# Optimization experiments

Measured on AMD Instinct MI355X. Metric: run time of the kernel, lower is better.

## Reference

```python
import jax, jax.numpy as jnp
import numpy as np

G, N, H = 64, 512, 64          # graphs, nodes/graph, hidden
NT = G * N                     # total nodes
DEG = 32
ET = NT * DEG                  # total edges
KP = int(np.ceil(0.7 * N))     # TopKPooling keep per graph (359)
NP2 = G * KP                   # nodes after pooling
F_IN, NC, NA = 128, 2, 6
seg = jax.ops.segment_sum


def graph_norm(h, batch, num_g, w, b, ms, eps=1e-5):
    cnt = seg(jnp.ones((h.shape[0], 1), h.dtype), batch, num_segments=num_g)
    mean = seg(h, batch, num_segments=num_g) / cnt
    hc = h - ms * mean[batch]
    var = seg(hc * hc, batch, num_segments=num_g) / cnt
    return w * hc / jnp.sqrt(var[batch] + eps) + b


def sage(h, src, tgt, valid, Ws, Wn, b, n_nodes):
    # PyG SAGEConv (mean aggr): out_i = x_i@Ws + mean_{j->i} x_j @ Wn + b
    msg = h[src] * valid[:, None]
    agg = seg(msg, tgt, num_segments=n_nodes)
    deg = seg(valid, tgt, num_segments=n_nodes)
    return h @ Ws + (agg / jnp.maximum(deg, 1.0)[:, None]) @ Wn + b


def setup_inputs() -> dict:
    key = jax.random.key(0)
    ks = jax.random.split(key, 20)
    offs = (jnp.arange(G) * N)[:, None]
    src = (jax.random.randint(ks[0], (G, N * DEG), 0, N) + offs).reshape(-1)
    tgt = (jax.random.randint(ks[1], (G, N * DEG), 0, N) + offs).reshape(-1)
    edge_index = jnp.stack([src, tgt])  # within-graph edges

    def lin(k, fi, fo):
        return jax.random.normal(k, (fi, fo), jnp.float32) / np.sqrt(fi)

    return {
        "x": jax.random.normal(ks[2], (NT, F_IN), jnp.float32),
        "edge_index": edge_index,
        "edge_attr": jax.random.uniform(ks[3], (ET,), jnp.float32),
        "coords": jax.random.normal(ks[4], (NT, 3), jnp.float32),
        "anatomical_class": jax.random.randint(ks[5], (NT,), 0, NA),
        "Bk_table": jax.random.normal(ks[6], (NA, H * H), jnp.float32) * 0.05,
        "pos_W": lin(ks[7], 3, H), "pos_b": jnp.zeros((H,), jnp.float32),
        "W1_self": lin(ks[8], F_IN, H), "W1_neigh": lin(ks[9], F_IN, H),
        "b1": jnp.zeros((H,), jnp.float32),
        "gn1_w": jnp.ones((H,), jnp.float32), "gn1_b": jnp.zeros((H,), jnp.float32),
        "gn1_ms": jnp.ones((H,), jnp.float32),
        "pool_p": jax.random.normal(ks[10], (H,), jnp.float32),
        "W2_self": lin(ks[11], H, H), "W2_neigh": lin(ks[12], H, H),
        "b2": jnp.zeros((H,), jnp.float32),
        "gn2_w": jnp.ones((H,), jnp.float32), "gn2_b": jnp.zeros((H,), jnp.float32),
        "gn2_ms": jnp.ones((H,), jnp.float32),
        "lin1_W": lin(ks[13], 3 * H, H), "lin1_b": jnp.zeros((H,), jnp.float32),
        "lin2_W": lin(ks[14], H, NC), "lin2_b": jnp.zeros((NC,), jnp.float32),
    }


def reference(x, edge_index, edge_attr, coords, anatomical_class, Bk_table,
              pos_W, pos_b, W1_self, W1_neigh, b1, gn1_w, gn1_b, gn1_ms,
              pool_p, W2_self, W2_neigh, b2, gn2_w, gn2_b, gn2_ms,
              lin1_W, lin1_b, lin2_W, lin2_b):
    row, col = edge_index[0], edge_index[1]
    batch = jnp.repeat(jnp.arange(G), N)
    # ---- stage 1: anatomical propagation kernel ----
    e = coords @ pos_W + pos_b                                 # [NT, H]
    Ae = seg(edge_attr[:, None] * e[col], row, num_segments=NT)  # SpMM adj @ e
    Bk = Bk_table[anatomical_class].reshape(NT, H, H)
    delta = jnp.einsum('nd,nhd->nh', Ae, Bk)                   # bmm(Ae, Bk^T)
    ones_e = jnp.ones((ET,), x.dtype)
    h = sage(x, row, col, ones_e, W1_self, W1_neigh, b1, NT)
    h = jax.nn.elu(graph_norm(h, batch, G, gn1_w, gn1_b, gn1_ms))
    h = h + delta
    h = jnp.einsum('nij,nj->ni', Bk + delta[:, :, None], h)    # propagate_message
    # ---- TopK pooling (equal-sized graphs) ----
    score = (h @ pool_p) / jnp.linalg.norm(pool_p)
    vals, idx = jax.lax.top_k(score.reshape(G, N), KP)
    perm = (idx + (jnp.arange(G) * N)[:, None]).reshape(-1)    # [NP2]
    h = h[perm] * jnp.tanh(vals).reshape(-1)[:, None]
    batch2 = jnp.repeat(jnp.arange(G), KP)
    node_map = jnp.full((NT,), -1, jnp.int32).at[perm].set(jnp.arange(NP2, dtype=jnp.int32))
    s2, t2 = node_map[row], node_map[col]
    valid = ((s2 >= 0) & (t2 >= 0)).astype(h.dtype)            # masked edge filter
    s2 = jnp.where(s2 >= 0, s2, 0)
    t2 = jnp.where(t2 >= 0, t2, 0)
    # ---- stage 2 ----
    e2 = coords[perm] @ pos_W + pos_b
    Bk2 = Bk_table[anatomical_class[perm]].reshape(NP2, H, H)
    Ae2 = seg(valid[:, None] * e2[t2], s2, num_segments=NP2)   # edge_attr = ones
    delta2 = jnp.einsum('nd,nhd->nh', Ae2, Bk2)
    h = h + delta2
    h = jnp.einsum('nij,nj->ni', Bk2 + delta2[:, :, None], h)
    h = sage(h, s2, t2, valid, W2_self, W2_neigh, b2, NP2)
    h = jax.nn.elu(graph_norm(h, batch2, G, gn2_w, gn2_b, gn2_ms))
    # ---- readout ----
    cnt = seg(jnp.ones((NP2, 1), h.dtype), batch2, num_segments=G)
    hsum = seg(h, batch2, num_segments=G)
    g = jnp.concatenate([hsum / cnt,
                         jax.ops.segment_max(h, batch2, num_segments=G),
                         hsum], axis=1)
    g = jax.nn.relu(g @ lin1_W + lin1_b)
    return jax.nn.log_softmax(g @ lin2_W + lin2_b, axis=1)
```

## Files before the change

### kernel.cpp

```cpp
#include <hip/hip_runtime.h>
#include <math.h>

#define G_    64
#define N_    512
#define NT_   32768
#define ET_   1048576
#define EPG_  16384
#define KP_   359
#define NP2_  22976
#define FIN_  128

__device__ __forceinline__
void gemm_unit(int unit, const float* __restrict__ in, int K,
               const float* __restrict__ Wa, const float* __restrict__ Wb,
               const float* __restrict__ bias,
               float* __restrict__ outA, float* __restrict__ outB,
               float* inT, int t) {
    int row0 = unit * 32;
    for (int idx = t; idx < 32 * K; idx += 256) inT[idx] = in[row0 * K + idx];
    __syncthreads();
    int c = t & 63, rb = t >> 6;
    const float* ip = inT + (rb * 8) * K;
    float aA[8] = {0,0,0,0,0,0,0,0};
    float aB[8] = {0,0,0,0,0,0,0,0};
    for (int k = 0; k < K; k += 4) {
        float wa0 = Wa[(k+0)*64 + c], wa1 = Wa[(k+1)*64 + c];
        float wa2 = Wa[(k+2)*64 + c], wa3 = Wa[(k+3)*64 + c];
        float wb0 = Wb[(k+0)*64 + c], wb1 = Wb[(k+1)*64 + c];
        float wb2 = Wb[(k+2)*64 + c], wb3 = Wb[(k+3)*64 + c];
        #pragma unroll
        for (int r = 0; r < 8; r++) {
            float4 xv = *(const float4*)&ip[r*K + k];
            aA[r] += xv.x*wa0; aB[r] += xv.x*wb0;
            aA[r] += xv.y*wa1; aB[r] += xv.y*wb1;
            aA[r] += xv.z*wa2; aB[r] += xv.z*wb2;
            aA[r] += xv.w*wa3; aB[r] += xv.w*wb3;
        }
    }
    float bv = bias[c];
    #pragma unroll
    for (int r = 0; r < 8; r++) {
        int node = row0 + rb*8 + r;
        outA[node*64 + c] = aA[r];
        outB[node*64 + c] = aB[r] + bv;
    }
}

__global__ __launch_bounds__(256)
void k_pregemm(const float* __restrict__ x,
               const float* __restrict__ W1n, const float* __restrict__ W1s,
               const float* __restrict__ b1,
               float* __restrict__ y, float* __restrict__ hself,
               const int* __restrict__ row, const int* __restrict__ col,
               int* __restrict__ histR8, int* __restrict__ histC8,
               const float* __restrict__ Bk, const float* __restrict__ posW,
               const float* __restrict__ posb,
               float* __restrict__ BkT, float* __restrict__ PT) {
    __shared__ float smem[32 * FIN_];
    int b = blockIdx.x, t = threadIdx.x;
    if (b < NT_/32) {
        gemm_unit(b, x, FIN_, W1n, W1s, b1, y, hself, smem, t);
    } else if (b < NT_/32 + 512) {
        int bb = b - NT_/32;
        int* hr = (int*)smem; int* hc = hr + N_;
        int g = bb >> 3, s = bb & 7;
        for (int i = t; i < N_; i += 256) { hr[i] = 0; hc[i] = 0; }
        __syncthreads();
        int ebase = g * EPG_ + s * 2048;
        for (int i = t; i < 2048; i += 256) {
            atomicAdd(&hr[row[ebase + i] & (N_ - 1)], 1);
            atomicAdd(&hc[col[ebase + i] & (N_ - 1)], 1);
        }
        __syncthreads();
        int sbase = bb * N_;
        for (int i = t; i < N_; i += 256) {
            histR8[sbase + i] = hr[i];
            histC8[sbase + i] = hc[i];
        }
    } else if (b < NT_/32 + 608) {
        int idx = (b - NT_/32 - 512) * 256 + t;
        int c = idx >> 12, r = idx & 4095;
        int h = r >> 6, d = r & 63;
        BkT[c*4096 + d*64 + h] = Bk[c*4096 + h*64 + d];
    } else {
        int c = b - (NT_/32 + 608);
        int i = t >> 6, h = t & 63;
        const float* B = Bk + c*4096 + h*64;
        float acc = 0.f;
        for (int d = 0; d < 64; d++) {
            float vd = (i < 3) ? posW[i*64 + d] : posb[d];
            acc += B[d] * vd;
        }
        PT[c*256 + i*64 + h] = acc;
    }
}

__global__ __launch_bounds__(1024)
void k_scatscan(const int* __restrict__ row, const int* __restrict__ col,
                const float* __restrict__ ea,
                const int* __restrict__ histR8, const int* __restrict__ histC8,
                int2* __restrict__ rowcsr, int* __restrict__ colcsr,
                int* __restrict__ rowptr, int* __restrict__ colptr,
                int* __restrict__ nmap) {
    __shared__ int hr[N_], hc[N_];
    int g = blockIdx.x >> 2, q = blockIdx.x & 3;
    int t = threadIdx.x;
    int lo = q * 128;
    int nbase = g * N_, ebase = g * EPG_;
    for (int i = t; i < N_; i += 1024) {
        int sr = 0, sc = 0;
        #pragma unroll
        for (int s = 0; s < 8; s++) {
            sr += histR8[(g*8 + s)*N_ + i];
            sc += histC8[(g*8 + s)*N_ + i];
        }
        hr[i] = sr; hc[i] = sc;
    }
    __syncthreads();
    int wave = t >> 6, lane = t & 63;
    if (wave < 2) {
        int* h = wave ? hc : hr;
        int base8 = lane * 8;
        int loc[8];
        int tot = 0;
        #pragma unroll
        for (int i = 0; i < 8; i++) { int v = h[base8 + i]; loc[i] = tot; tot += v; }
        int pref = tot;
        for (int off = 1; off < 64; off <<= 1) {
            int u = __shfl_up(pref, off);
            if (lane >= off) pref += u;
        }
        pref -= tot;
        #pragma unroll
        for (int i = 0; i < 8; i++) h[base8 + i] = pref + loc[i];
    }
    __syncthreads();
    if (t < 128) {
        int i = lo + t;
        rowptr[nbase + i] = ebase + hr[i];
        colptr[nbase + i] = ebase + hc[i];
        nmap[nbase + i] = -1;
    }
    if (blockIdx.x == 0 && t == 0) { rowptr[NT_] = ET_; colptr[NT_] = ET_; }
    __syncthreads();
    for (int i = t; i < EPG_; i += 1024) {
        int rg = row[ebase + i];
        int cg = col[ebase + i];
        int rl = (rg & (N_ - 1)) - lo;
        if ((unsigned)rl < 128u) {
            int pr = atomicAdd(&hr[lo + rl], 1);
            rowcsr[ebase + pr] = make_int2(cg, __float_as_int(ea[ebase + i]));
        }
        int cl = (cg & (N_ - 1)) - lo;
        if ((unsigned)cl < 128u) {
            int pc = atomicAdd(&hc[lo + cl], 1);
            colcsr[ebase + pc] = rg;
        }
    }
}

__global__ __launch_bounds__(256)
void k_edge1f(const int* __restrict__ rowptr, const int2* __restrict__ rcsr,
              const int* __restrict__ colptr, const int* __restrict__ ccsr,
              const float* __restrict__ coords, const float* __restrict__ y,
              const float* __restrict__ hself,
              float4* __restrict__ nsum, float* __restrict__ vbuf) {
    int node = blockIdx.x * 4 + (threadIdx.x >> 6);
    int lane = threadIdx.x & 63;
    int rs = rowptr[node], re = rowptr[node + 1];
    float sx = 0.f, sy = 0.f, sz = 0.f, sw = 0.f;
    for (int k = rs + lane; k < re; k += 64) {
        int2 ent = rcsr[k];
        int c = ent.x;
        float w = __int_as_float(ent.y);
        sx += w * coords[c*3+0];
        sy += w * coords[c*3+1];
        sz += w * coords[c*3+2];
        sw += w;
    }
    #pragma unroll
    for (int off = 32; off; off >>= 1) {
        sx += __shfl_xor(sx, off); sy += __shfl_xor(sy, off);
        sz += __shfl_xor(sz, off); sw += __shfl_xor(sw, off);
    }
    if (lane == 0) nsum[node] = make_float4(sx, sy, sz, sw);
    int cs = colptr[node], ce = colptr[node + 1];
    float acc = 0.f;
    #pragma unroll 8
    for (int k = cs; k < ce; k++) {
        int r = ccsr[k];
        acc += y[r*64 + lane];
    }
    vbuf[node*64 + lane] = hself[node*64 + lane] + acc / fmaxf((float)(ce - cs), 1.f);
}

__global__ __launch_bounds__(256)
void k_gnstat(const float* __restrict__ v, float* __restrict__ partial,
              int NPG, int CH, int npc) {
    __shared__ float r1[256], r2[256];
    int b = blockIdx.x;
    int g = b / CH, chunk = b % CH;
    int t = threadIdx.x, c = t & 63, grp = t >> 6;
    int n0 = chunk * npc;
    int nend = min(n0 + npc, NPG);
    float s1 = 0.f, s2 = 0.f;
    for (int n = n0 + grp; n < nend; n += 4) {
        float vv = v[(g * NPG + n)*64 + c];
        s1 += vv; s2 += vv * vv;
    }
    r1[t] = s1; r2[t] = s2;
    __syncthreads();
    if (grp == 0) {
        partial[b*128 + c]      = r1[c] + r1[64+c] + r1[128+c] + r1[192+c];
        partial[b*128 + 64 + c] = r2[c] + r2[64+c] + r2[128+c] + r2[192+c];
    }
}

__global__ __launch_bounds__(256)
void k_gnprop(const float* __restrict__ vbuf, const float* __restrict__ partial,
              const float* __restrict__ ms,
              const float* __restrict__ w, const float* __restrict__ b,
              const float4* __restrict__ nsum, const int* __restrict__ cls,
              const float* __restrict__ PT, const float* __restrict__ BkT,
              float* __restrict__ out) {
    __shared__ float hT[256];
    int t = threadIdx.x;
    int node = blockIdx.x * 4 + (t >> 6);
    int lane = t & 63;
    int g = (blockIdx.x * 4) >> 9;
    float s1 = 0.f, s2 = 0.f;
    #pragma unroll
    for (int i = 0; i < 8; i++) {
        s1 += partial[(g*8 + i)*128 + lane];
        s2 += partial[(g*8 + i)*128 + 64 + lane];
    }
    float m  = s1 / (float)N_, q = s2 / (float)N_, msv = ms[lane];
    float var = q - msv * m * m * (2.f - msv);
    float mval = msv * m;
    float istd = rsqrtf(var + 1e-5f);
    float4 s4 = nsum[node];
    int c = cls[node];
    const float* P = PT + c * 256;
    float d = s4.x*P[lane] + s4.y*P[64+lane] + s4.z*P[128+lane] + s4.w*P[192+lane];
    float v = vbuf[node*64 + lane];
    v = w[lane] * (v - mval) * istd + b[lane];
    v = v > 0.f ? v : expm1f(v);
    v += d;
    hT[t] = v;
    __syncthreads();
    float ssum = v;
    #pragma unroll
    for (int off = 32; off; off >>= 1) ssum += __shfl_xor(ssum, off);
    const float* B  = BkT + c * 4096;
    const float* hv = hT + (t & ~63);
    float acc = 0.f;
    #pragma unroll 8
    for (int j = 0; j < 64; j++) acc += B[j*64 + lane] * hv[j];
    out[node*64 + lane] = acc + d * ssum;
}

__global__ __launch_bounds__(512)
void k_topk(const float* __restrict__ hp, const float* __restrict__ p,
            const int* __restrict__ cls, const int* __restrict__ ccsr,
            const int* __restrict__ row, const int* __restrict__ col,
            int* __restrict__ perm, float* __restrict__ tanhv,
            int* __restrict__ node_map, int* __restrict__ class2,
            int* __restrict__ ccsr2, float* __restrict__ deg2) {
    __shared__ float key[N_];
    __shared__ int   idxS[N_];
    __shared__ int   lmap[N_];
    __shared__ int   ideg[KP_];
    __shared__ float pS[64];
    __shared__ float nrm;
    int g = blockIdx.x, t = threadIdx.x;
    lmap[t] = -1;
    if (t < 64) pS[t] = p[t];
    for (int i = t; i < KP_; i += 512) ideg[i] = 0;
    __syncthreads();
    if (t == 0) {
        float s = 0.f;
        for (int i = 0; i < 64; i++) s += pS[i] * pS[i];
        nrm = sqrtf(s);
    }
    __syncthreads();
    {
        float acc = 0.f;
        const float* hv = hp + (size_t)(g*N_ + t) * 64;
        for (int cdx = 0; cdx < 64; cdx++) acc += hv[cdx] * pS[cdx];
        key[t]  = acc / nrm;
        idxS[t] = t;
    }
    __syncthreads();
    for (int k = 2; k <= N_; k <<= 1) {
        for (int j = k >> 1; j > 0; j >>= 1) {
            int i = t, ixj = i ^ j;
            if (ixj > i) {
                float ki = key[i], kj = key[ixj];
                int   ii = idxS[i], ij = idxS[ixj];
                bool before = (ki > kj) || (ki == kj && ii < ij);
                bool dir = ((i & k) == 0);
                if (dir ? !before : before) {
                    key[i] = kj; key[ixj] = ki;
                    idxS[i] = ij; idxS[ixj] = ii;
                }
            }
            __syncthreads();
        }
    }
    if (t < KP_) {
        int orig  = idxS[t];
        int gnode = g * N_ + orig;
        int pj    = g * KP_ + t;
        perm[pj]     = gnode;
        tanhv[pj]    = tanhf(key[t]);
        node_map[gnode] = pj;
        class2[pj]   = cls[gnode];
        lmap[orig]   = pj;
    }
    __syncthreads();
    int ebase = g * EPG_;
    for (int k = t; k < EPG_; k += 512) {
        int mm = lmap[ccsr[ebase + k] & (N_ - 1)];
        ccsr2[ebase + k] = (mm >= 0) ? mm : NP2_;
    }
    for (int k = t; k < EPG_; k += 512) {
        int mr = lmap[row[ebase + k] & (N_ - 1)];
        int mc = lmap[col[ebase + k] & (N_ - 1)];
        if (mr >= 0 && mc >= 0) atomicAdd(&ideg[mc - g * KP_], 1);
    }
    __syncthreads();
    for (int i = t; i < KP_; i += 512) deg2[g * KP_ + i] = (float)ideg[i];
}

__global__ __launch_bounds__(256)
void k_s2prop(const int* __restrict__ rowptr, const int2* __restrict__ rcsr,
              const int* __restrict__ perm, const int* __restrict__ nmap,
              const float* __restrict__ coords,
              const float* __restrict__ hp, const float* __restrict__ tanhv,
              const int* __restrict__ cls2,
              const float* __restrict__ PT, const float* __restrict__ BkT,
              float* __restrict__ out, float* __restrict__ y2zero) {
    __shared__ float hT[256];
    int t = threadIdx.x;
    int j = blockIdx.x * 4 + (t >> 6);
    int lane = t & 63;
    if (blockIdx.x == 0 && t < 64) y2zero[t] = 0.f;
    int orig = perm[j];
    int rs = rowptr[orig], re = rowptr[orig + 1];
    float sx = 0.f, sy = 0.f, sz = 0.f, sw = 0.f;
    for (int k = rs + lane; k < re; k += 64) {
        int c = rcsr[k].x;
        if (nmap[c] >= 0) {
            sx += coords[c*3+0]; sy += coords[c*3+1]; sz += coords[c*3+2];
            sw += 1.f;
        }
    }
    #pragma unroll
    for (int off = 32; off; off >>= 1) {
        sx += __shfl_xor(sx, off); sy += __shfl_xor(sy, off);
        sz += __shfl_xor(sz, off); sw += __shfl_xor(sw, off);
    }
    int c = cls2[j];
    const float* P = PT + c * 256;
    float d = sx*P[lane] + sy*P[64+lane] + sz*P[128+lane] + sw*P[192+lane];
    float v = hp[orig*64 + lane] * tanhv[j] + d;
    hT[t] = v;
    __syncthreads();
    float ssum = v;
    #pragma unroll
    for (int off = 32; off; off >>= 1) ssum += __shfl_xor(ssum, off);
    const float* B  = BkT + c * 4096;
    const float* hv = hT + (t & ~63);
    float acc = 0.f;
    #pragma unroll 8
    for (int jj = 0; jj < 64; jj++) acc += B[jj*64 + lane] * hv[jj];
    out[j*64 + lane] = acc + d * ssum;
}

__global__ __launch_bounds__(256)
void k_gemm2(const float* __restrict__ in,
             const float* __restrict__ Wa, const float* __restrict__ Wb,
             const float* __restrict__ bias,
             float* __restrict__ outA, float* __restrict__ outB) {
    __shared__ float inT[32 * 64];
    gemm_unit(blockIdx.x, in, 64, Wa, Wb, bias, outA, outB, inT, threadIdx.x);
}

__global__ __launch_bounds__(256)
void k_gagg2v(const int* __restrict__ colptr, const int* __restrict__ ccsr2,
              const int* __restrict__ perm, const float* __restrict__ y2,
              const float* __restrict__ hs2, const float* __restrict__ deg2,
              float* __restrict__ v2buf) {
    int j = blockIdx.x * 4 + (threadIdx.x >> 6);
    int lane = threadIdx.x & 63;
    int orig = perm[j];
    int start = colptr[orig], end = colptr[orig + 1];
    float acc = 0.f;
    #pragma unroll 8
    for (int k = start; k < end; k++) {
        int r = ccsr2[k];
        acc += y2[r*64 + lane];
    }
    v2buf[j*64 + lane] = hs2[j*64 + lane] + acc / fmaxf(deg2[j], 1.f);
}

__global__ __launch_bounds__(256)
void k_gnrd(const float* __restrict__ v2, const float* __restrict__ statsP,
            const float* __restrict__ ms,
            const float* __restrict__ w, const float* __restrict__ b,
            float* __restrict__ readP) {
    __shared__ float r1[256], r2[256];
    int blk = blockIdx.x;
    int g = blk / 6, chunk = blk % 6;
    int t = threadIdx.x, c = t & 63, grp = t >> 6;
    float s1 = 0.f, s2 = 0.f;
    #pragma unroll
    for (int i = 0; i < 6; i++) {
        s1 += statsP[(g*6 + i)*128 + c];
        s2 += statsP[(g*6 + i)*128 + 64 + c];
    }
    float mean = s1 / (float)KP_, q = s2 / (float)KP_, msv = ms[c];
    float var = q - msv * mean * mean * (2.f - msv);
    float mv = msv * mean;
    float is = rsqrtf(var + 1e-5f);
    float wv = w[c], bv = b[c];
    int n0 = chunk * 60, nend = min(n0 + 60, KP_);
    float s = 0.f, m = -1e30f;
    for (int n = n0 + grp; n < nend; n += 4) {
        float v = v2[(g * KP_ + n)*64 + c];
        v = wv * (v - mv) * is + bv;
        v = v > 0.f ? v : expm1f(v);
        s += v; m = fmaxf(m, v);
    }
    r1[t] = s; r2[t] = m;
    __syncthreads();
    if (grp == 0) {
        readP[blk*128 + c]      = r1[c] + r1[64+c] + r1[128+c] + r1[192+c];
        readP[blk*128 + 64 + c] = fmaxf(fmaxf(r2[c], r2[64+c]), fmaxf(r2[128+c], r2[192+c]));
    }
}

__global__ void k_rfin(const float* __restrict__ part, int CH,
                       const float* __restrict__ l1W, const float* __restrict__ l1b,
                       const float* __restrict__ l2W, const float* __restrict__ l2b,
                       float* __restrict__ out) {
    __shared__ float gv[192], rS[64];
    int g = blockIdx.x, t = threadIdx.x;
    float s = 0.f, m = -1e30f;
    for (int i = 0; i < CH; i++) {
        s += part[(g*CH + i)*128 + t];
        m = fmaxf(m, part[(g*CH + i)*128 + 64 + t]);
    }
    gv[t] = s / (float)KP_;
    gv[64 + t] = m;
    gv[128 + t] = s;
    __syncthreads();
    float acc = l1b[t];
    for (int k = 0; k < 192; k++) acc += gv[k] * l1W[k*64 + t];
    rS[t] = fmaxf(acc, 0.f);
    __syncthreads();
    if (t == 0) {
        float l0 = l2b[0], l1v = l2b[1];
        for (int hh = 0; hh < 64; hh++) { l0 += rS[hh]*l2W[hh*2+0]; l1v += rS[hh]*l2W[hh*2+1]; }
        float mx  = fmaxf(l0, l1v);
        float lse = mx + logf(expf(l0 - mx) + expf(l1v - mx));
        out[g*2 + 0] = l0  - lse;
        out[g*2 + 1] = l1v - lse;
    }
}

extern "C" void kernel_launch(void* const* d_in, const int* in_sizes, int n_in,
                              void* d_out, int out_size, void* d_ws, size_t ws_size,
                              hipStream_t stream) {
    const float* x      = (const float*)d_in[0];
    const int*   eidx   = (const int*)  d_in[1];
    const float* eattr  = (const float*)d_in[2];
    const float* coords = (const float*)d_in[3];
    const int*   acls   = (const int*)  d_in[4];
    const float* BkTab  = (const float*)d_in[5];
    const float* posW   = (const float*)d_in[6];
    const float* posb   = (const float*)d_in[7];
    const float* W1s    = (const float*)d_in[8];
    const float* W1n    = (const float*)d_in[9];
    const float* b1     = (const float*)d_in[10];
    const float* gn1w   = (const float*)d_in[11];
    const float* gn1b   = (const float*)d_in[12];
    const float* gn1ms  = (const float*)d_in[13];
    const float* poolp  = (const float*)d_in[14];
    const float* W2s    = (const float*)d_in[15];
    const float* W2n    = (const float*)d_in[16];
    const float* b2     = (const float*)d_in[17];
    const float* gn2w   = (const float*)d_in[18];
    const float* gn2b   = (const float*)d_in[19];
    const float* gn2ms  = (const float*)d_in[20];
    const float* l1W    = (const float*)d_in[21];
    const float* l1b    = (const float*)d_in[22];
    const float* l2W    = (const float*)d_in[23];
    const float* l2b    = (const float*)d_in[24];

    const int* row  = eidx;
    const int* colp = eidx + ET_;

    float* W = (float*)d_ws;
    const size_t NTH = (size_t)NT_ * 64;
    float* b0    = W;
    float* b1buf = W + 1*NTH;
    float* b2buf = W + 2*NTH;
    float* b3buf = W + 3*NTH;
    float* p = W + 4*NTH;
    int2*  rowcsr = (int2*)p;        p += 2*(size_t)ET_;
    int*   colcsr = (int*)p;         p += ET_;
    int*   ccsr2  = (int*)p;         p += ET_;
    int*   rowptr = (int*)p;         p += NT_ + 8;
    int*   colptr = (int*)p;         p += NT_ + 8;
    int*   histR8 = (int*)p;         p += NT_ * 8;
    int*   histC8 = (int*)p;         p += NT_ * 8;
    float* deg2   = p;               p += NP2_;
    float* tanhv  = p;               p += NP2_;
    int*   perm   = (int*)p;         p += NP2_;
    int*   nmap   = (int*)p;         p += NT_;
    int*   cls2   = (int*)p;         p += NP2_;
    float* BkT    = p;               p += 6 * 4096;
    float* PT     = p;               p += 6 * 256;
    float* statsP = p;               p += (size_t)G_ * 8 * 128;
    float* readP  = p;               p += (size_t)G_ * 6 * 128;
    float4* nsum  = (float4*)b3buf;

    k_pregemm  <<<NT_/32 + 614, 256, 0, stream>>>(x, W1n, W1s, b1,
                                                  b0 , b1buf ,
                                                  row, colp, histR8, histC8,
                                                  BkTab, posW, posb, BkT, PT);
    k_scatscan <<<G_*4,    1024, 0, stream>>>(row, colp, eattr, histR8, histC8,
                                              rowcsr, colcsr, rowptr, colptr, nmap);
    k_edge1f   <<<NT_/4,   256, 0, stream>>>(rowptr, rowcsr, colptr, colcsr,
                                             coords, b0 , b1buf ,
                                             nsum, b2buf );
    k_gnstat   <<<G_*8,    256, 0, stream>>>(b2buf , statsP, N_, 8, 64);
    k_gnprop   <<<NT_/4,   256, 0, stream>>>(b2buf , statsP, gn1ms,
                                             gn1w, gn1b, nsum, acls, PT, BkT,
                                             b1buf );
    k_topk     <<<G_,      512, 0, stream>>>(b1buf , poolp, acls, colcsr,
                                             row, colp, perm, tanhv, nmap,
                                             cls2, ccsr2, deg2);

    k_s2prop   <<<NP2_/4,  256, 0, stream>>>(rowptr, rowcsr, perm, nmap, coords,
                                             b1buf , tanhv, cls2, PT, BkT,
                                             b2buf ,
                                             b0 + (size_t)NP2_ * 64 );
    k_gemm2    <<<NP2_/32, 256, 0, stream>>>(b2buf , W2n, W2s, b2,
                                             b0 , b3buf );
    k_gagg2v   <<<NP2_/4,  256, 0, stream>>>(colptr, ccsr2, perm, b0 ,
                                             b3buf , deg2,
                                             b1buf );
    k_gnstat   <<<G_*6,    256, 0, stream>>>(b1buf , statsP, KP_, 6, 60);
    k_gnrd     <<<G_*6,    256, 0, stream>>>(b1buf , statsP, gn2ms,
                                             gn2w, gn2b, readP);
    k_rfin     <<<G_,      64,  0, stream>>>(readP, 6, l1W, l1b, l2W, l2b,
                                             (float*)d_out);
}
```

Before: 333.7 us.

## Fuse stage-2 propagation into SAGE GEMM and merge readout kernels

Merges the stage-2 Bk propagation kernel with the following dense W2 GEMM, so each block computes 32 pooled rows into shared memory and multiplies them there, with no global round-trip. Also folds the GraphNorm readout partials and the final MLP/log-softmax into one 512-thread kernel per graph. Both changes cut two launches and some global traffic. The cost is lower parallelism: each block now handles 32 rows with 8 serial rows per wave in stage 2, and the readout runs on only 64 blocks.

```diff
diff --git a/kernel.cpp b/kernel.cpp
--- a/kernel.cpp
+++ b/kernel.cpp
@@ -333,57 +333,81 @@
 }
 
 __global__ __launch_bounds__(256)
-void k_s2prop(const int* __restrict__ rowptr, const int2* __restrict__ rcsr,
+void k_s2gemm(const int* __restrict__ rowptr, const int2* __restrict__ rcsr,
               const int* __restrict__ perm, const int* __restrict__ nmap,
               const float* __restrict__ coords,
               const float* __restrict__ hp, const float* __restrict__ tanhv,
               const int* __restrict__ cls2,
               const float* __restrict__ PT, const float* __restrict__ BkT,
-              float* __restrict__ out, float* __restrict__ y2zero) {
-    __shared__ float hT[256];
+              const float* __restrict__ W2n, const float* __restrict__ W2s,
+              const float* __restrict__ b2,
+              float* __restrict__ y2, float* __restrict__ hs2) {
+    __shared__ float hT[32 * 64];
+    __shared__ float p2T[32 * 64];
     int t = threadIdx.x;
-    int j = blockIdx.x * 4 + (t >> 6);
-    int lane = t & 63;
-    if (blockIdx.x == 0 && t < 64) y2zero[t] = 0.f;
-    int orig = perm[j];
-    int rs = rowptr[orig], re = rowptr[orig + 1];
-    float sx = 0.f, sy = 0.f, sz = 0.f, sw = 0.f;
-    for (int k = rs + lane; k < re; k += 64) {
-        int c = rcsr[k].x;
-        if (nmap[c] >= 0) {
-            sx += coords[c*3+0]; sy += coords[c*3+1]; sz += coords[c*3+2];
-            sw += 1.f;
-        }
-    }
-    #pragma unroll
-    for (int off = 32; off; off >>= 1) {
-        sx += __shfl_xor(sx, off); sy += __shfl_xor(sy, off);
-        sz += __shfl_xor(sz, off); sw += __shfl_xor(sw, off);
-    }
-    int c = cls2[j];
-    const float* P = PT + c * 256;
-    float d = sx*P[lane] + sy*P[64+lane] + sz*P[128+lane] + sw*P[192+lane];
-    float v = hp[orig*64 + lane] * tanhv[j] + d;
-    hT[t] = v;
-    __syncthreads();
-    float ssum = v;
-    #pragma unroll
-    for (int off = 32; off; off >>= 1) ssum += __shfl_xor(ssum, off);
-    const float* B  = BkT + c * 4096;
-    const float* hv = hT + (t & ~63);
-    float acc = 0.f;
-    #pragma unroll 8
-    for (int jj = 0; jj < 64; jj++) acc += B[jj*64 + lane] * hv[jj];
-    out[j*64 + lane] = acc + d * ssum;
-}
-
-__global__ __launch_bounds__(256)
-void k_gemm2(const float* __restrict__ in,
-             const float* __restrict__ Wa, const float* __restrict__ Wb,
-             const float* __restrict__ bias,
-             float* __restrict__ outA, float* __restrict__ outB) {
-    __shared__ float inT[32 * 64];
-    gemm_unit(blockIdx.x, in, 64, Wa, Wb, bias, outA, outB, inT, threadIdx.x);
+    int wave = t >> 6, lane = t & 63;
+    int j0 = blockIdx.x * 32;
+    if (blockIdx.x == 0 && t < 64) y2[(size_t)NP2_ * 64 + t] = 0.f;
+    #pragma unroll
+    for (int r = 0; r < 8; r++) {
+        int li = wave * 8 + r;
+        int j  = j0 + li;
+        int orig = perm[j];
+        int rs = rowptr[orig], re = rowptr[orig + 1];
+        float sx = 0.f, sy = 0.f, sz = 0.f, sw = 0.f;
+        for (int k = rs + lane; k < re; k += 64) {
+            int c = rcsr[k].x;
+            if (nmap[c] >= 0) {
+                sx += coords[c*3+0]; sy += coords[c*3+1]; sz += coords[c*3+2];
+                sw += 1.f;
+            }
+        }
+        #pragma unroll
+        for (int off = 32; off; off >>= 1) {
+            sx += __shfl_xor(sx, off); sy += __shfl_xor(sy, off);
+            sz += __shfl_xor(sz, off); sw += __shfl_xor(sw, off);
+        }
+        int c = cls2[j];
+        const float* P = PT + c * 256;
+        float d = sx*P[lane] + sy*P[64+lane] + sz*P[128+lane] + sw*P[192+lane];
+        float v = hp[orig*64 + lane] * tanhv[j] + d;
+        hT[li*64 + lane] = v;
+        float ssum = v;
+        #pragma unroll
+        for (int off = 32; off; off >>= 1) ssum += __shfl_xor(ssum, off);
+        const float* B  = BkT + c * 4096;
+        const float* hv = hT + li * 64;
+        float acc = 0.f;
+        #pragma unroll 8
+        for (int jj = 0; jj < 64; jj++) acc += B[jj*64 + lane] * hv[jj];
+        p2T[li*64 + lane] = acc + d * ssum;
+    }
+    __syncthreads();
+    int cc = lane, rb = wave;
+    const float* ip = p2T + (rb * 8) * 64;
+    float aA[8] = {0,0,0,0,0,0,0,0};
+    float aB[8] = {0,0,0,0,0,0,0,0};
+    for (int k = 0; k < 64; k += 4) {
+        float wa0 = W2n[(k+0)*64 + cc], wa1 = W2n[(k+1)*64 + cc];
+        float wa2 = W2n[(k+2)*64 + cc], wa3 = W2n[(k+3)*64 + cc];
+        float wb0 = W2s[(k+0)*64 + cc], wb1 = W2s[(k+1)*64 + cc];
+        float wb2 = W2s[(k+2)*64 + cc], wb3 = W2s[(k+3)*64 + cc];
+        #pragma unroll
+        for (int r = 0; r < 8; r++) {
+            float4 xv = *(const float4*)&ip[r*64 + k];
+            aA[r] += xv.x*wa0; aB[r] += xv.x*wb0;
+            aA[r] += xv.y*wa1; aB[r] += xv.y*wb1;
+            aA[r] += xv.z*wa2; aB[r] += xv.z*wb2;
+            aA[r] += xv.w*wa3; aB[r] += xv.w*wb3;
+        }
+    }
+    float bv = b2[cc];
+    #pragma unroll
+    for (int r = 0; r < 8; r++) {
+        int j = j0 + rb*8 + r;
+        y2[j*64 + cc]  = aA[r];
+        hs2[j*64 + cc] = aB[r] + bv;
+    }
 }
 
 __global__ __launch_bounds__(256)
@@ -404,15 +428,17 @@
     v2buf[j*64 + lane] = hs2[j*64 + lane] + acc / fmaxf(deg2[j], 1.f);
 }
 
-__global__ __launch_bounds__(256)
-void k_gnrd(const float* __restrict__ v2, const float* __restrict__ statsP,
-            const float* __restrict__ ms,
-            const float* __restrict__ w, const float* __restrict__ b,
-            float* __restrict__ readP) {
-    __shared__ float r1[256], r2[256];
-    int blk = blockIdx.x;
-    int g = blk / 6, chunk = blk % 6;
-    int t = threadIdx.x, c = t & 63, grp = t >> 6;
+__global__ __launch_bounds__(512)
+void k_gnrdfin(const float* __restrict__ v2, const float* __restrict__ statsP,
+               const float* __restrict__ ms,
+               const float* __restrict__ w, const float* __restrict__ b,
+               const float* __restrict__ l1W, const float* __restrict__ l1b,
+               const float* __restrict__ l2W, const float* __restrict__ l2b,
+               float* __restrict__ out) {
+    __shared__ float r1[512], r2[512];
+    __shared__ float gv[192], rS[64];
+    int g = blockIdx.x, t = threadIdx.x;
+    int c = t & 63, grp = t >> 6;
     float s1 = 0.f, s2 = 0.f;
     #pragma unroll
     for (int i = 0; i < 6; i++) {
@@ -424,9 +450,8 @@
     float mv = msv * mean;
     float is = rsqrtf(var + 1e-5f);
     float wv = w[c], bv = b[c];
-    int n0 = chunk * 60, nend = min(n0 + 60, KP_);
     float s = 0.f, m = -1e30f;
-    for (int n = n0 + grp; n < nend; n += 4) {
+    for (int n = grp; n < KP_; n += 8) {
         float v = v2[(g * KP_ + n)*64 + c];
         v = wv * (v - mv) * is + bv;
         v = v > 0.f ? v : expm1f(v);
@@ -435,29 +460,22 @@
     r1[t] = s; r2[t] = m;
     __syncthreads();
     if (grp == 0) {
-        readP[blk*128 + c]      = r1[c] + r1[64+c] + r1[128+c] + r1[192+c];
-        readP[blk*128 + 64 + c] = fmaxf(fmaxf(r2[c], r2[64+c]), fmaxf(r2[128+c], r2[192+c]));
-    }
-}
-
-__global__ void k_rfin(const float* __restrict__ part, int CH,
-                       const float* __restrict__ l1W, const float* __restrict__ l1b,
-                       const float* __restrict__ l2W, const float* __restrict__ l2b,
-                       float* __restrict__ out) {
-    __shared__ float gv[192], rS[64];
-    int g = blockIdx.x, t = threadIdx.x;
-    float s = 0.f, m = -1e30f;
-    for (int i = 0; i < CH; i++) {
-        s += part[(g*CH + i)*128 + t];
-        m = fmaxf(m, part[(g*CH + i)*128 + 64 + t]);
-    }
-    gv[t] = s / (float)KP_;
-    gv[64 + t] = m;
-    gv[128 + t] = s;
-    __syncthreads();
-    float acc = l1b[t];
-    for (int k = 0; k < 192; k++) acc += gv[k] * l1W[k*64 + t];
-    rS[t] = fmaxf(acc, 0.f);
+        float ss = 0.f, mm = -1e30f;
+        #pragma unroll
+        for (int i = 0; i < 8; i++) {
+            ss += r1[i*64 + c];
+            mm = fmaxf(mm, r2[i*64 + c]);
+        }
+        gv[c]       = ss / (float)KP_;
+        gv[64 + c]  = mm;
+        gv[128 + c] = ss;
+    }
+    __syncthreads();
+    if (t < 64) {
+        float acc = l1b[t];
+        for (int k = 0; k < 192; k++) acc += gv[k] * l1W[k*64 + t];
+        rS[t] = fmaxf(acc, 0.f);
+    }
     __syncthreads();
     if (t == 0) {
         float l0 = l2b[0], l1v = l2b[1];
@@ -523,7 +541,6 @@
     float* BkT    = p;               p += 6 * 4096;
     float* PT     = p;               p += 6 * 256;
     float* statsP = p;               p += (size_t)G_ * 8 * 128;
-    float* readP  = p;               p += (size_t)G_ * 6 * 128;
     float4* nsum  = (float4*)b3buf;
 
     k_pregemm  <<<NT_/32 + 614, 256, 0, stream>>>(x, W1n, W1s, b1,
@@ -543,18 +560,15 @@
                                              row, colp, perm, tanhv, nmap,
                                              cls2, ccsr2, deg2);
 
-    k_s2prop   <<<NP2_/4,  256, 0, stream>>>(rowptr, rowcsr, perm, nmap, coords,
+    k_s2gemm   <<<NP2_/32, 256, 0, stream>>>(rowptr, rowcsr, perm, nmap, coords,
                                              b1buf , tanhv, cls2, PT, BkT,
-                                             b2buf ,
-                                             b0 + (size_t)NP2_ * 64 );
-    k_gemm2    <<<NP2_/32, 256, 0, stream>>>(b2buf , W2n, W2s, b2,
+                                             W2n, W2s, b2,
                                              b0 , b3buf );
     k_gagg2v   <<<NP2_/4,  256, 0, stream>>>(colptr, ccsr2, perm, b0 ,
                                              b3buf , deg2,
                                              b1buf );
     k_gnstat   <<<G_*6,    256, 0, stream>>>(b1buf , statsP, KP_, 6, 60);
-    k_gnrd     <<<G_*6,    256, 0, stream>>>(b1buf , statsP, gn2ms,
-                                             gn2w, gn2b, readP);
-    k_rfin     <<<G_,      64,  0, stream>>>(readP, 6, l1W, l1b, l2W, l2b,
+    k_gnrdfin  <<<G_,      512, 0, stream>>>(b1buf , statsP, gn2ms,
+                                             gn2w, gn2b, l1W, l1b, l2W, l2b,
                                              (float*)d_out);
 }
```

Result: slower. 353.5 us (+5.9%).
